# Kernel optimization log

Measured on AMD Instinct MI355X. Metric: run time of the kernel, lower is better.

## Reference

```python
import jax, jax.numpy as jnp
import numpy as np

B, S, D = 1, 2048, 4096
H = 32
Q_RANK, KV_RANK = 1536, 512
NOPE, ROPE, VD = 128, 64, 128
QD = NOPE + ROPE  # 192
EPS = 1e-6
THETA = 10000.0


def setup_inputs() -> dict:
    key = jax.random.key(0)
    ks = jax.random.split(key, 8)
    std = 0.02
    return {
        'hidden_states': jax.random.normal(ks[0], (B, S, D), jnp.float32),
        'Wq_a': jax.random.normal(ks[1], (D, Q_RANK), jnp.float32) * std,
        'q_a_ln_w': jnp.ones((Q_RANK,), jnp.float32),
        'Wq_b': jax.random.normal(ks[2], (Q_RANK, H * QD), jnp.float32) * std,
        'Wkv_a': jax.random.normal(ks[3], (D, KV_RANK + ROPE), jnp.float32) * std,
        'kv_a_ln_w': jnp.ones((KV_RANK,), jnp.float32),
        'Wkv_b': jax.random.normal(ks[4], (KV_RANK, H * (NOPE + VD)), jnp.float32) * std,
        'Wo': jax.random.normal(ks[5], (H * VD, D), jnp.float32) * std,
    }


def _rmsnorm(x, w):
    return x * jax.lax.rsqrt(jnp.mean(x * x, axis=-1, keepdims=True) + EPS) * w


def _rotate_half(x):
    h = x.shape[-1] // 2
    return jnp.concatenate([-x[..., h:], x[..., :h]], axis=-1)


def _apply_rope(x, cos, sin):
    # DeepSeek interleave permutation: view(..., d//2, 2).transpose -> [evens | odds]
    xp = jnp.concatenate([x[..., 0::2], x[..., 1::2]], axis=-1)
    return xp * cos + _rotate_half(xp) * sin


def _mla_forward(hidden_states, Wq_a, q_a_ln_w, Wq_b, Wkv_a, kv_a_ln_w, Wkv_b, Wo):
    b, s, _ = hidden_states.shape
    # low-rank query projection
    q = _rmsnorm(hidden_states @ Wq_a, q_a_ln_w) @ Wq_b          # [b,s,H*QD]
    q = q.reshape(b, s, H, QD).transpose(0, 2, 1, 3)             # [b,H,s,QD]
    q_nope, q_pe = q[..., :NOPE], q[..., NOPE:]
    # compressed kv + shared rope key
    ckv = hidden_states @ Wkv_a                                   # [b,s,KV_RANK+ROPE]
    compressed, k_pe = ckv[..., :KV_RANK], ckv[..., KV_RANK:]
    kv = _rmsnorm(compressed, kv_a_ln_w) @ Wkv_b                 # [b,s,H*(NOPE+VD)]
    kv = kv.reshape(b, s, H, NOPE + VD).transpose(0, 2, 1, 3)    # [b,H,s,NOPE+VD]
    k_nope, v = kv[..., :NOPE], kv[..., NOPE:]
    k_pe = k_pe[:, None, :, :]                                    # [b,1,s,ROPE]
    # rotary tables (cos/sin duplicated halves)
    inv_freq = 1.0 / (THETA ** (jnp.arange(0, ROPE, 2, dtype=jnp.float32) / ROPE))
    freqs = jnp.outer(jnp.arange(s, dtype=jnp.float32), inv_freq)  # [s,ROPE/2]
    emb = jnp.concatenate([freqs, freqs], axis=-1)                 # [s,ROPE]
    cos = jnp.cos(emb)[None, None].astype(hidden_states.dtype)
    sin = jnp.sin(emb)[None, None].astype(hidden_states.dtype)
    q_pe = _apply_rope(q_pe, cos, sin)
    k_pe = _apply_rope(k_pe, cos, sin)
    # assemble full q/k heads
    qf = jnp.concatenate([q_nope, q_pe], axis=-1)                 # [b,H,s,QD]
    kf = jnp.concatenate([k_nope, jnp.broadcast_to(k_pe, (b, H, s, ROPE))], axis=-1)
    scale = QD ** (-0.5)
    scores = jnp.einsum('bhqd,bhkd->bhqk', qf, kf) * scale        # [b,H,s,s]
    causal = jnp.tril(jnp.ones((s, s), dtype=bool))
    scores = jnp.where(causal, scores, jnp.finfo(scores.dtype).min)
    probs = jax.nn.softmax(scores, axis=-1)
    o = jnp.einsum('bhqk,bhkd->bhqd', probs, v)                   # [b,H,s,VD]
    o = o.transpose(0, 2, 1, 3).reshape(b, s, H * VD)
    return o @ Wo


def reference(hidden_states, Wq_a, q_a_ln_w, Wq_b, Wkv_a, kv_a_ln_w, Wkv_b, Wo):
    return _mla_forward(hidden_states, Wq_a, q_a_ln_w, Wq_b, Wkv_a, kv_a_ln_w, Wkv_b, Wo)
```

## Files before the change

### kernel.cpp

```cpp
#include <hip/hip_runtime.h>

typedef unsigned short u16;
using bf16x8 = __attribute__((ext_vector_type(8))) __bf16;
using f32x4  = __attribute__((ext_vector_type(4))) float;
using s16x8  = __attribute__((ext_vector_type(8))) short;
using s16x4  = __attribute__((ext_vector_type(4))) short;

#define AS1 __attribute__((address_space(1)))
#define AS3 __attribute__((address_space(3)))

__device__ __forceinline__ void gload16(const u16* g, u16* l) {
  __builtin_amdgcn_global_load_lds((AS1 void*)(size_t)g, (AS3 void*)l, 16, 0, 0);
}

__device__ __forceinline__ u16 f2bf(float f) {
  unsigned u = __float_as_uint(f);
  u += 0x7fffu + ((u >> 16) & 1u);
  return (u16)(u >> 16);
}
__device__ __forceinline__ float bf2f(u16 h) {
  return __uint_as_float(((unsigned)h) << 16);
}

__device__ __forceinline__ void transpose_tile(const float* __restrict__ W,
                                               u16* __restrict__ WT,
                                               int K, int N, int nb, int kb,
                                               u16 (*tile)[72]) {
  const int t = threadIdx.x;
  const int rr = t >> 3;
  const int cc = (t & 7) * 8;
#pragma unroll
  for (int pass = 0; pass < 2; ++pass) {
    const float* src = W + (size_t)(kb + pass * 32 + rr) * N + nb + cc;
    float4 a = *reinterpret_cast<const float4*>(src);
    float4 b = *reinterpret_cast<const float4*>(src + 4);
    u16* tr = &tile[pass * 32 + rr][cc];
    tr[0] = f2bf(a.x); tr[1] = f2bf(a.y); tr[2] = f2bf(a.z); tr[3] = f2bf(a.w);
    tr[4] = f2bf(b.x); tr[5] = f2bf(b.y); tr[6] = f2bf(b.z); tr[7] = f2bf(b.w);
  }
  __syncthreads();
#pragma unroll
  for (int pass = 0; pass < 2; ++pass) {
    s16x8 v;
#pragma unroll
    for (int j = 0; j < 8; ++j) v[j] = (short)tile[cc + j][pass * 32 + rr];
    *reinterpret_cast<s16x8*>(WT + (size_t)(nb + pass * 32 + rr) * K + kb + cc) = v;
  }
}

__global__ __launch_bounds__(256) void prep_merged_kernel(
    const float* __restrict__ hs, u16* __restrict__ hs_bf,
    const float* __restrict__ Wqa, const float* __restrict__ Wkva, u16* __restrict__ WabT,
    const float* __restrict__ Wqb, u16* __restrict__ WqbT,
    const float* __restrict__ Wkvb, u16* __restrict__ WkvbT,
    const float* __restrict__ Wo, u16* __restrict__ WoT,
    float* __restrict__ cost, float* __restrict__ sint) {
  __shared__ u16 tile[64][72];
  const int bid = blockIdx.x, t = threadIdx.x;
  if (bid < 8192) {
    int i = (bid * 256 + t) * 4;
    float4 v = *reinterpret_cast<const float4*>(hs + i);
    s16x4 o;
    o[0] = (short)f2bf(v.x); o[1] = (short)f2bf(v.y);
    o[2] = (short)f2bf(v.z); o[3] = (short)f2bf(v.w);
    *reinterpret_cast<s16x4*>(hs_bf + i) = o;
  } else if (bid < 9728) {
    int r = bid - 8192;
    transpose_tile(Wqa, WabT, 4096, 1536, (r % 24) * 64, (r / 24) * 64, tile);
  } else if (bid < 10304) {
    int r = bid - 9728;
    transpose_tile(Wkva, WabT + (size_t)1536 * 4096, 4096, 576, (r % 9) * 64, (r / 9) * 64, tile);
  } else if (bid < 12608) {
    int r = bid - 10304;
    transpose_tile(Wqb, WqbT, 1536, 6144, (r % 96) * 64, (r / 96) * 64, tile);
  } else if (bid < 13632) {
    int r = bid - 12608;
    transpose_tile(Wkvb, WkvbT, 512, 8192, (r % 128) * 64, (r / 128) * 64, tile);
  } else if (bid < 17728) {
    int r = bid - 13632;
    transpose_tile(Wo, WoT, 4096, 4096, (r % 64) * 64, (r / 64) * 64, tile);
  } else {
    int idx = (bid - 17728) * 256 + t;
    int pos = idx >> 5, j = idx & 31;
    float inv = __expf(-(float)j * (9.210340371976184f / 32.0f));
    float f = (float)pos * inv;
    cost[idx] = cosf(f);
    sint[idx] = sinf(f);
  }
}

__global__ __launch_bounds__(256) void norms_merged_kernel(const u16* __restrict__ fused,
                                                           const float* __restrict__ qln,
                                                           const float* __restrict__ kvln,
                                                           u16* __restrict__ qan,
                                                           u16* __restrict__ cn) {
  const int bid = blockIdx.x, t = threadIdx.x;
  const int row = bid & 2047;
  const bool is_q = bid < 2048;
  const int R = is_q ? 1536 : 512;
  const u16* xr = fused + (size_t)row * 2112 + (is_q ? 0 : 1536);
  const float* w = is_q ? qln : kvln;
  u16* yr = (is_q ? qan + (size_t)row * 1536 : cn + (size_t)row * 512);
  float ss = 0.f;
  for (int i = t; i < R; i += 256) { float f = bf2f(xr[i]); ss += f * f; }
#pragma unroll
  for (int m = 32; m >= 1; m >>= 1) ss += __shfl_xor(ss, m);
  __shared__ float red[4];
  if ((t & 63) == 0) red[t >> 6] = ss;
  __syncthreads();
  float tot = red[0] + red[1] + red[2] + red[3];
  float r = rsqrtf(tot / (float)R + 1e-6f);
  for (int i = t; i < R; i += 256) yr[i] = f2bf(bf2f(xr[i]) * r * w[i]);
}

__global__ __launch_bounds__(256) void builds_merged_kernel(const u16* __restrict__ q,
                                                            const u16* __restrict__ ckv,
                                                            const float* __restrict__ cost,
                                                            const float* __restrict__ sint,
                                                            u16* __restrict__ qf,
                                                            u16* __restrict__ kf) {
  const int bid = blockIdx.x, t = threadIdx.x;
  if (bid < 6144) {
    int o8 = (bid * 256 + t) * 8;
    const float scale = 0.07216878364870323f;
    int c = (o8 % 192) >> 3;
    int rest = o8 / 192;
    int s = rest & 2047, h = rest >> 11;
    const u16* qrow = q + ((size_t)s * 32 + h) * 192;
    s16x8 out;
    if (c < 16) {
      s16x8 v = *reinterpret_cast<const s16x8*>(qrow + c * 8);
#pragma unroll
      for (int j = 0; j < 8; ++j) out[j] = (short)f2bf(bf2f((u16)v[j]) * scale);
    } else {
      int j0 = c * 8 - 128;
      bool lo = j0 < 32;
      int jj0 = lo ? j0 : j0 - 32;
      s16x8 a = *reinterpret_cast<const s16x8*>(qrow + 128 + 2 * jj0);
      s16x8 b = *reinterpret_cast<const s16x8*>(qrow + 128 + 2 * jj0 + 8);
      float4 c0 = *reinterpret_cast<const float4*>(cost + s * 32 + jj0);
      float4 c1 = *reinterpret_cast<const float4*>(cost + s * 32 + jj0 + 4);
      float4 s0 = *reinterpret_cast<const float4*>(sint + s * 32 + jj0);
      float4 s1 = *reinterpret_cast<const float4*>(sint + s * 32 + jj0 + 4);
      float cs[8] = {c0.x, c0.y, c0.z, c0.w, c1.x, c1.y, c1.z, c1.w};
      float sn[8] = {s0.x, s0.y, s0.z, s0.w, s1.x, s1.y, s1.z, s1.w};
#pragma unroll
      for (int j = 0; j < 8; ++j) {
        float x0 = bf2f((u16)((j < 4) ? a[2 * j] : b[2 * j - 8]));
        float x1 = bf2f((u16)((j < 4) ? a[2 * j + 1] : b[2 * j - 7]));
        float v = lo ? (x0 * cs[j] - x1 * sn[j]) : (x1 * cs[j] + x0 * sn[j]);
        out[j] = (short)f2bf(v * scale);
      }
    }
    *reinterpret_cast<s16x8*>(qf + o8) = out;
  } else {
    int o8 = ((bid - 6144) * 256 + t) * 8;
    int j0 = o8 & 63;
    int rest = o8 >> 6;
    int s = rest & 2047, h = rest >> 11;
    bool lo = j0 < 32;
    int jj0 = lo ? j0 : j0 - 32;
    const u16* crow = ckv + (size_t)s * 2112 + 512;
    s16x8 a = *reinterpret_cast<const s16x8*>(crow + 2 * jj0);
    s16x8 b = *reinterpret_cast<const s16x8*>(crow + 2 * jj0 + 8);
    float4 c0 = *reinterpret_cast<const float4*>(cost + s * 32 + jj0);
    float4 c1 = *reinterpret_cast<const float4*>(cost + s * 32 + jj0 + 4);
    float4 s0 = *reinterpret_cast<const float4*>(sint + s * 32 + jj0);
    float4 s1 = *reinterpret_cast<const float4*>(sint + s * 32 + jj0 + 4);
    float cs[8] = {c0.x, c0.y, c0.z, c0.w, c1.x, c1.y, c1.z, c1.w};
    float sn[8] = {s0.x, s0.y, s0.z, s0.w, s1.x, s1.y, s1.z, s1.w};
    s16x8 out;
#pragma unroll
    for (int j = 0; j < 8; ++j) {
      float x0 = bf2f((u16)((j < 4) ? a[2 * j] : b[2 * j - 8]));
      float x1 = bf2f((u16)((j < 4) ? a[2 * j + 1] : b[2 * j - 7]));
      float v = lo ? (x0 * cs[j] - x1 * sn[j]) : (x1 * cs[j] + x0 * sn[j]);
      out[j] = (short)f2bf(v);
    }
    *reinterpret_cast<s16x8*>(kf + ((size_t)h * 2048 + s) * 192 + 128 + j0) = out;
  }
}

template <int EPI>
__device__ __forceinline__ void gemm_v3_body(const u16* __restrict__ A,
                                             const u16* __restrict__ BT,
                                             void* __restrict__ Cv,
                                             void* __restrict__ Cv2,
                                             int M, int N, int K,
                                             int bx, int by, u16* S) {
  const int t0 = threadIdx.x;
  const int lane = t0 & 63, wave = t0 >> 6;
  const int wr = wave >> 1, wc = wave & 1;
  const int row0 = by * 128, col0 = bx * 128;
  const int lrow = lane & 15, lkg = lane >> 4;

  const int lp = lane ^ ((lane >> 3) & 3);
  const int srow_off = lp >> 2;
  const int skel = (lp & 3) * 8;
  const int c0 = wave * 2, c1 = c0 + 1;
  const int arow_c0 = row0 + c0 * 16 + srow_off;
  const int arow_c1 = row0 + c1 * 16 + srow_off;
  int brow_c0 = col0 + c0 * 16 + srow_off; if (brow_c0 > N - 1) brow_c0 = N - 1;
  int brow_c1 = col0 + c1 * 16 + srow_off; if (brow_c1 > N - 1) brow_c1 = N - 1;

  int aoff[4], boff[4];
#pragma unroll
  for (int m = 0; m < 4; ++m) {
    int r = wr * 64 + m * 16 + lrow;
    int off = r * 32 + lkg * 8;
    aoff[m] = off ^ ((off >> 3) & 0x18);
    r = wc * 64 + m * 16 + lrow;
    off = r * 32 + lkg * 8;
    boff[m] = off ^ ((off >> 3) & 0x18);
  }

  const int NT = K >> 5;

#pragma unroll
  for (int pt = 0; pt < 3; ++pt) {
    u16* ab = &S[pt * 8192];
    const int kb = pt * 32 + skel;
    gload16(A  + (size_t)arow_c0 * K + kb, ab + c0 * 512);
    gload16(A  + (size_t)arow_c1 * K + kb, ab + c1 * 512);
    gload16(BT + (size_t)brow_c0 * K + kb, ab + 4096 + c0 * 512);
    gload16(BT + (size_t)brow_c1 * K + kb, ab + 4096 + c1 * 512);
  }

  f32x4 acc[4][4];
#pragma unroll
  for (int m = 0; m < 4; ++m)
#pragma unroll
    for (int n = 0; n < 4; ++n) acc[m][n] = 0.f;

  for (int t = 0; t < NT; ++t) {
    if (t + 2 < NT)      asm volatile("s_waitcnt vmcnt(8)" ::: "memory");
    else if (t + 1 < NT) asm volatile("s_waitcnt vmcnt(4)" ::: "memory");
    else                 asm volatile("s_waitcnt vmcnt(0)" ::: "memory");
    __builtin_amdgcn_s_barrier();
    __builtin_amdgcn_sched_barrier(0);

    const u16* ab = &S[(t & 3) * 8192];
    bf16x8 af[4], bb[4];
#pragma unroll
    for (int m = 0; m < 4; ++m)
      af[m] = *reinterpret_cast<const bf16x8*>(ab + aoff[m]);
#pragma unroll
    for (int n = 0; n < 4; ++n)
      bb[n] = *reinterpret_cast<const bf16x8*>(ab + 4096 + boff[n]);

    if (t + 3 < NT) {
      u16* sb = &S[((t + 3) & 3) * 8192];
      const int kb = (t + 3) * 32 + skel;
      gload16(A  + (size_t)arow_c0 * K + kb, sb + c0 * 512);
      gload16(A  + (size_t)arow_c1 * K + kb, sb + c1 * 512);
      gload16(BT + (size_t)brow_c0 * K + kb, sb + 4096 + c0 * 512);
      gload16(BT + (size_t)brow_c1 * K + kb, sb + 4096 + c1 * 512);
    }

    __builtin_amdgcn_s_setprio(1);
#pragma unroll
    for (int m = 0; m < 4; ++m)
#pragma unroll
      for (int n = 0; n < 4; ++n)
        acc[m][n] = __builtin_amdgcn_mfma_f32_16x16x32_bf16(af[m], bb[n], acc[m][n], 0, 0, 0);
    __builtin_amdgcn_s_setprio(0);
  }

#pragma unroll
  for (int m = 0; m < 4; ++m) {
#pragma unroll
    for (int n = 0; n < 4; ++n) {
      int col = col0 + wc * 64 + n * 16 + lrow;
      int row = row0 + wr * 64 + m * 16 + lkg * 4;
      if (col < N) {
#pragma unroll
        for (int i = 0; i < 4; ++i) {
          size_t idx = (size_t)(row + i) * N + col;
          if (EPI == 1) ((u16*)Cv)[idx] = f2bf(acc[m][n][i]);
          else          ((float*)Cv)[idx] = acc[m][n][i];
        }
      }
    }
  }
}

template <int EPI>
__global__ __launch_bounds__(256) void gemm_v3_kernel(const u16* __restrict__ A,
                                                      const u16* __restrict__ BT,
                                                      void* __restrict__ Cv,
                                                      void* __restrict__ Cv2,
                                                      int M, int N, int K) {
  __shared__ __align__(16) u16 S[4 * 8192];
  gemm_v3_body<EPI>(A, BT, Cv, Cv2, M, N, K, blockIdx.x, blockIdx.y, S);
}

template <int EPI>
__device__ __forceinline__ void gemm_v4_body(const u16* __restrict__ A,
                                             const u16* __restrict__ BT,
                                             void* __restrict__ Cv,
                                             void* __restrict__ Cv2,
                                             int M, int N, int K,
                                             int bx, int by, u16* S) {
  const int t0 = threadIdx.x;
  const int lane = t0 & 63, wave = t0 >> 6;
  const int wr = wave >> 1, wc = wave & 1;
  const int row0 = by * 128, col0 = bx * 256;
  const int lrow = lane & 15, lkg = lane >> 4;

  const int lp = lane ^ ((lane >> 3) & 3);
  const int srow_off = lp >> 2;
  const int skel = (lp & 3) * 8;

  const int ac0 = wave * 2, ac1 = ac0 + 1;
  const int arow_0 = row0 + ac0 * 16 + srow_off;
  const int arow_1 = row0 + ac1 * 16 + srow_off;
  int brow[4];
#pragma unroll
  for (int j = 0; j < 4; ++j) {
    int r = col0 + (wave * 4 + j) * 16 + srow_off;
    brow[j] = (r > N - 1) ? (N - 1) : r;
  }

  int aoff[4], boff[8];
#pragma unroll
  for (int m = 0; m < 4; ++m) {
    int r = wr * 64 + m * 16 + lrow;
    int off = r * 32 + lkg * 8;
    aoff[m] = off ^ ((off >> 3) & 0x18);
  }
#pragma unroll
  for (int n = 0; n < 8; ++n) {
    int r = wc * 128 + n * 16 + lrow;
    int off = r * 32 + lkg * 8;
    boff[n] = off ^ ((off >> 3) & 0x18);
  }

  const int NT = K >> 5;

#pragma unroll
  for (int pt = 0; pt < 2; ++pt) {
    u16* sb = &S[pt * 12288];
    const int kb = pt * 32 + skel;
    gload16(A + (size_t)arow_0 * K + kb, sb + ac0 * 512);
    gload16(A + (size_t)arow_1 * K + kb, sb + ac1 * 512);
#pragma unroll
    for (int j = 0; j < 4; ++j)
      gload16(BT + (size_t)brow[j] * K + kb, sb + 4096 + (wave * 4 + j) * 512);
  }

  f32x4 acc[4][8];
#pragma unroll
  for (int m = 0; m < 4; ++m)
#pragma unroll
    for (int n = 0; n < 8; ++n) acc[m][n] = 0.f;

  int bufr = 0, bufw = 2;
  for (int t = 0; t < NT; ++t) {
    if (t + 2 < NT) {
      u16* sb = &S[bufw * 12288];
      const int kb = (t + 2) * 32 + skel;
      gload16(A + (size_t)arow_0 * K + kb, sb + ac0 * 512);
      gload16(A + (size_t)arow_1 * K + kb, sb + ac1 * 512);
#pragma unroll
      for (int j = 0; j < 4; ++j)
        gload16(BT + (size_t)brow[j] * K + kb, sb + 4096 + (wave * 4 + j) * 512);
      bufw = (bufw + 1 == 3) ? 0 : bufw + 1;
      asm volatile("s_waitcnt vmcnt(12)" ::: "memory");
    } else if (t + 1 < NT) {
      asm volatile("s_waitcnt vmcnt(6)" ::: "memory");
    } else {
      asm volatile("s_waitcnt vmcnt(0)" ::: "memory");
    }
    __builtin_amdgcn_s_barrier();
    __builtin_amdgcn_sched_barrier(0);

    const u16* ab = &S[bufr * 12288];
    bufr = (bufr + 1 == 3) ? 0 : bufr + 1;
    bf16x8 af[4];
#pragma unroll
    for (int m = 0; m < 4; ++m)
      af[m] = *reinterpret_cast<const bf16x8*>(ab + aoff[m]);

    __builtin_amdgcn_s_setprio(1);
#pragma unroll
    for (int n = 0; n < 8; ++n) {
      bf16x8 bbn = *reinterpret_cast<const bf16x8*>(ab + 4096 + boff[n]);
#pragma unroll
      for (int m = 0; m < 4; ++m)
        acc[m][n] = __builtin_amdgcn_mfma_f32_16x16x32_bf16(af[m], bbn, acc[m][n], 0, 0, 0);
    }
    __builtin_amdgcn_s_setprio(0);
  }

#pragma unroll
  for (int m = 0; m < 4; ++m) {
#pragma unroll
    for (int n = 0; n < 8; ++n) {
      int col = col0 + wc * 128 + n * 16 + lrow;
      int row = row0 + wr * 64 + m * 16 + lkg * 4;
      if (EPI == 2) {
        int d = col & 255, hh = col >> 8;
        if (d < 128) {
          u16* dst = (u16*)Cv + ((size_t)hh * 2048 + row) * 192 + d;
#pragma unroll
          for (int i = 0; i < 4; ++i) dst[(size_t)i * 192] = f2bf(acc[m][n][i]);
        } else {
          s16x4 v;
#pragma unroll
          for (int i = 0; i < 4; ++i) v[i] = (short)f2bf(acc[m][n][i]);
          *reinterpret_cast<s16x4*>((u16*)Cv2 + ((size_t)hh * 128 + (d - 128)) * 2048 + row) = v;
        }
      } else if (col < N) {
#pragma unroll
        for (int i = 0; i < 4; ++i) {
          size_t idx = (size_t)(row + i) * N + col;
          if (EPI == 1) ((u16*)Cv)[idx] = f2bf(acc[m][n][i]);
          else          ((float*)Cv)[idx] = acc[m][n][i];
        }
      }
    }
  }
}

template <int EPI>
__global__ __launch_bounds__(256, 2) void gemm_v4_kernel(const u16* __restrict__ A,
                                                         const u16* __restrict__ BT,
                                                         void* __restrict__ Cv,
                                                         void* __restrict__ Cv2,
                                                         int M, int N, int K) {
  __shared__ __align__(16) u16 S[3 * 12288];
  gemm_v4_body<EPI>(A, BT, Cv, Cv2, M, N, K, blockIdx.x, blockIdx.y, S);
}

__global__ __launch_bounds__(256, 2) void gemm_qkv_kernel(const u16* __restrict__ qan,
                                                          const u16* __restrict__ WqbT,
                                                          u16* __restrict__ qout,
                                                          const u16* __restrict__ cn,
                                                          const u16* __restrict__ WkvbT,
                                                          u16* __restrict__ kfb,
                                                          u16* __restrict__ vTb) {
  __shared__ __align__(16) u16 S[3 * 12288];
  if (blockIdx.z == 0) {
    if (blockIdx.x >= 24) return;
    gemm_v4_body<1>(qan, WqbT, qout, nullptr, 2048, 6144, 1536, blockIdx.x, blockIdx.y, S);
  } else {
    gemm_v4_body<2>(cn, WkvbT, kfb, vTb, 2048, 8192, 512, blockIdx.x, blockIdx.y, S);
  }
}

__global__ __launch_bounds__(256) void mla_attn_kernel(const u16* __restrict__ qf,
                                                       const u16* __restrict__ kf,
                                                       const u16* __restrict__ vT,
                                                       u16* __restrict__ o) {
  const int h = blockIdx.x, pair = blockIdx.y;
  const int t = threadIdx.x, wave = t >> 6, lane = t & 63;
  const int lrow = lane & 15, lkg = lane >> 4;
  __shared__ __align__(16) u16 Kt[2][12 * 512];
  __shared__ __align__(16) u16 Vt[2][8 * 512];
  __shared__ __align__(16) u16 Pl[4][16][36];

  const u16* ksrc[3]; u16 *kdst0[3], *kdst1[3];
#pragma unroll
  for (int i = 0; i < 3; ++i) {
    int c = wave * 3 + i, cg = c / 6, kk = c - cg * 6;
    ksrc[i] = kf + ((size_t)h * 2048 + cg * 16 + lrow) * 192 + kk * 32 + lkg * 8;
    kdst0[i] = &Kt[0][c * 512];
    kdst1[i] = &Kt[1][c * 512];
  }
  const u16* vsrc[2]; u16 *vdst0[2], *vdst1[2];
#pragma unroll
  for (int j = 0; j < 2; ++j) {
    int f = wave * 2 + j;
    vsrc[j] = vT + ((size_t)h * 128 + f * 16 + lrow) * 2048 + lkg * 8;
    vdst0[j] = &Vt[0][f * 512];
    vdst1[j] = &Vt[1][f * 512];
  }

  for (int qq = 0; qq < 2; ++qq) {
    const int qb = qq ? (31 - pair) : pair;
    const int qbase = qb * 64 + wave * 16;

    bf16x8 qfr[6];
    const u16* qrow_ptr = qf + ((size_t)h * 2048 + qbase + lrow) * 192;
#pragma unroll
    for (int kk = 0; kk < 6; ++kk)
      qfr[kk] = *reinterpret_cast<const bf16x8*>(qrow_ptr + kk * 32 + lkg * 8);

    f32x4 acc_o[8];
#pragma unroll
    for (int f = 0; f < 8; ++f) acc_o[f] = 0.f;
    float m_run[4], l_par[4];
#pragma unroll
    for (int i = 0; i < 4; ++i) { m_run[i] = -1e30f; l_par[i] = 0.f; }

    const int nt = 2 * qb + 2;

#pragma unroll
    for (int i = 0; i < 3; ++i) gload16(ksrc[i], kdst0[i]);
#pragma unroll
    for (int j = 0; j < 2; ++j) gload16(vsrc[j], vdst0[j]);

    for (int it = 0; it < nt; ++it) {
      const int kt = it * 32;
      if (it + 1 < nt) {
        const int nb = (it + 1) & 1;
        const size_t kadv = (size_t)(it + 1) * 32 * 192;
        const size_t vadv = (size_t)(it + 1) * 32;
#pragma unroll
        for (int i = 0; i < 3; ++i) gload16(ksrc[i] + kadv, nb ? kdst1[i] : kdst0[i]);
#pragma unroll
        for (int j = 0; j < 2; ++j) gload16(vsrc[j] + vadv, nb ? vdst1[j] : vdst0[j]);
        asm volatile("s_waitcnt vmcnt(5)" ::: "memory");
      } else {
        asm volatile("s_waitcnt vmcnt(0)" ::: "memory");
      }
      __builtin_amdgcn_s_barrier();
      __builtin_amdgcn_sched_barrier(0);

      const u16* Kb = &Kt[it & 1][0];
      const u16* Vb = &Vt[it & 1][0];
      if (kt <= qbase + 15) {
        f32x4 sv[2];
        sv[0] = 0.f; sv[1] = 0.f;
#pragma unroll
        for (int cg = 0; cg < 2; ++cg)
#pragma unroll
          for (int kk = 0; kk < 6; ++kk) {
            bf16x8 kfr = *reinterpret_cast<const bf16x8*>(&Kb[(cg * 6 + kk) * 512 + lane * 8]);
            sv[cg] = __builtin_amdgcn_mfma_f32_16x16x32_bf16(qfr[kk], kfr, sv[cg], 0, 0, 0);
          }
        const int qrow_b = qbase + lkg * 4;
        if (kt + 31 > qbase) {
#pragma unroll
          for (int cg = 0; cg < 2; ++cg) {
            int kvcol = kt + cg * 16 + lrow;
#pragma unroll
            for (int i = 0; i < 4; ++i)
              if (kvcol > qrow_b + i) sv[cg][i] = -__builtin_inff();
          }
        }
        float tmax[4];
#pragma unroll
        for (int i = 0; i < 4; ++i) tmax[i] = fmaxf(sv[0][i], sv[1][i]);
#pragma unroll
        for (int m = 8; m >= 1; m >>= 1)
#pragma unroll
          for (int i = 0; i < 4; ++i) tmax[i] = fmaxf(tmax[i], __shfl_xor(tmax[i], m));
        int need = 0;
#pragma unroll
        for (int i = 0; i < 4; ++i) need |= (tmax[i] > m_run[i] + 8.f) ? 1 : 0;
        if (__any(need)) {
#pragma unroll
          for (int i = 0; i < 4; ++i) {
            float mnew = fmaxf(m_run[i], tmax[i]);
            float alpha = __expf(m_run[i] - mnew);
            m_run[i] = mnew;
            l_par[i] *= alpha;
#pragma unroll
            for (int f = 0; f < 8; ++f) acc_o[f][i] *= alpha;
          }
        }
#pragma unroll
        for (int i = 0; i < 4; ++i) {
          sv[0][i] = __expf(sv[0][i] - m_run[i]);
          sv[1][i] = __expf(sv[1][i] - m_run[i]);
          l_par[i] += sv[0][i] + sv[1][i];
        }
#pragma unroll
        for (int cg = 0; cg < 2; ++cg)
#pragma unroll
          for (int i = 0; i < 4; ++i)
            Pl[wave][lkg * 4 + i][cg * 16 + lrow] = f2bf(sv[cg][i]);
        bf16x8 pf = *reinterpret_cast<const bf16x8*>(&Pl[wave][lrow][lkg * 8]);
#pragma unroll
        for (int f = 0; f < 8; ++f) {
          bf16x8 vfr = *reinterpret_cast<const bf16x8*>(&Vb[f * 512 + lane * 8]);
          acc_o[f] = __builtin_amdgcn_mfma_f32_16x16x32_bf16(pf, vfr, acc_o[f], 0, 0, 0);
        }
      }
      __builtin_amdgcn_sched_barrier(0);
      __builtin_amdgcn_s_barrier();
    }
#pragma unroll
    for (int i = 0; i < 4; ++i)
#pragma unroll
      for (int m = 8; m >= 1; m >>= 1) l_par[i] += __shfl_xor(l_par[i], m);
#pragma unroll
    for (int f = 0; f < 8; ++f)
#pragma unroll
      for (int i = 0; i < 4; ++i) {
        int row = qbase + lkg * 4 + i;
        int col = h * 128 + f * 16 + lrow;
        o[(size_t)row * 4096 + col] = f2bf(acc_o[f][i] / l_par[i]);
      }
  }
}

extern "C" void kernel_launch(void* const* d_in, const int* in_sizes, int n_in,
                              void* d_out, int out_size, void* d_ws, size_t ws_size,
                              hipStream_t stream) {
  (void)in_sizes; (void)n_in; (void)out_size; (void)ws_size;
  const float* hs   = (const float*)d_in[0];
  const float* Wqa  = (const float*)d_in[1];
  const float* qln  = (const float*)d_in[2];
  const float* Wqb  = (const float*)d_in[3];
  const float* Wkva = (const float*)d_in[4];
  const float* kvln = (const float*)d_in[5];
  const float* Wkvb = (const float*)d_in[6];
  const float* Wo   = (const float*)d_in[7];
  float* out = (float*)d_out;

  char* p = (char*)d_ws;
  size_t off = 0;
  auto carve = [&](size_t bytes) {
    char* r = p + off;
    off += (bytes + 255) & ~(size_t)255;
    return r;
  };
  u16* hs_bf = (u16*)carve((size_t)2048 * 4096 * 2);
  u16* WabT  = (u16*)carve((size_t)2112 * 4096 * 2);
  u16* WqbT  = (u16*)carve((size_t)6144 * 1536 * 2);
  u16* WkvbT = (u16*)carve((size_t)8192 * 512 * 2);
  u16* WoT   = (u16*)carve((size_t)4096 * 4096 * 2);
  u16* fused = (u16*)carve((size_t)2048 * 2112 * 2);
  u16* qan   = (u16*)carve((size_t)2048 * 1536 * 2);
  u16* q     = (u16*)carve((size_t)2048 * 6144 * 2);
  u16* cn    = (u16*)carve((size_t)2048 * 512 * 2);
  u16* qfb   = (u16*)carve((size_t)32 * 2048 * 192 * 2);
  u16* kfb   = (u16*)carve((size_t)32 * 2048 * 192 * 2);
  u16* vTb   = (u16*)carve((size_t)32 * 128 * 2048 * 2);
  u16* ob    = (u16*)carve((size_t)2048 * 4096 * 2);
  float* cost = (float*)carve((size_t)65536 * 4);
  float* sint = (float*)carve((size_t)65536 * 4);

  prep_merged_kernel<<<17984, 256, 0, stream>>>(hs, hs_bf, Wqa, Wkva, WabT,
                                                Wqb, WqbT, Wkvb, WkvbT, Wo, WoT,
                                                cost, sint);

  gemm_v3_kernel<1><<<dim3(17, 16), 256, 0, stream>>>(hs_bf, WabT, fused, nullptr, 2048, 2112, 4096);

  norms_merged_kernel<<<4096, 256, 0, stream>>>(fused, qln, kvln, qan, cn);

  gemm_qkv_kernel<<<dim3(32, 16, 2), 256, 0, stream>>>(qan, WqbT, q, cn, WkvbT, kfb, vTb);

  builds_merged_kernel<<<8192, 256, 0, stream>>>(q, fused + 1536, cost, sint, qfb, kfb);

  mla_attn_kernel<<<dim3(32, 16), 256, 0, stream>>>(qfb, kfb, vTb, ob);

  gemm_v4_kernel<0><<<dim3(16, 16), 256, 0, stream>>>(ob, WoT, out, nullptr, 2048, 4096, 4096);
}
```

Before: 399.1 us.

## Enlarge attention KV tile to 64 and single-buffer V with late prefetch

After: 393.3 us (median of 2 runs). No clear change (-1.5%).

```diff
diff --git a/kernel.cpp b/kernel.cpp
--- a/kernel.cpp
+++ b/kernel.cpp
@@ -455,26 +455,12 @@
   const int h = blockIdx.x, pair = blockIdx.y;
   const int t = threadIdx.x, wave = t >> 6, lane = t & 63;
   const int lrow = lane & 15, lkg = lane >> 4;
-  __shared__ __align__(16) u16 Kt[2][12 * 512];
-  __shared__ __align__(16) u16 Vt[2][8 * 512];
-  __shared__ __align__(16) u16 Pl[4][16][36];
-
-  const u16* ksrc[3]; u16 *kdst0[3], *kdst1[3];
-#pragma unroll
-  for (int i = 0; i < 3; ++i) {
-    int c = wave * 3 + i, cg = c / 6, kk = c - cg * 6;
-    ksrc[i] = kf + ((size_t)h * 2048 + cg * 16 + lrow) * 192 + kk * 32 + lkg * 8;
-    kdst0[i] = &Kt[0][c * 512];
-    kdst1[i] = &Kt[1][c * 512];
-  }
-  const u16* vsrc[2]; u16 *vdst0[2], *vdst1[2];
-#pragma unroll
-  for (int j = 0; j < 2; ++j) {
-    int f = wave * 2 + j;
-    vsrc[j] = vT + ((size_t)h * 128 + f * 16 + lrow) * 2048 + lkg * 8;
-    vdst0[j] = &Vt[0][f * 512];
-    vdst1[j] = &Vt[1][f * 512];
-  }
+  __shared__ __align__(16) u16 Kt[2][24 * 512];
+  __shared__ __align__(16) u16 Vt[16 * 512];
+  __shared__ __align__(16) u16 Pl[4][16][72];
+
+  const u16* ksrc0 = kf + ((size_t)h * 2048 + wave * 16 + lrow) * 192 + lkg * 8;
+  const u16* vsrc0 = vT + ((size_t)h * 128 + wave * 32 + lrow) * 2048 + lkg * 8;
 
   for (int qq = 0; qq < 2; ++qq) {
     const int qb = qq ? (31 - pair) : pair;
@@ -493,24 +479,27 @@
 #pragma unroll
     for (int i = 0; i < 4; ++i) { m_run[i] = -1e30f; l_par[i] = 0.f; }
 
-    const int nt = 2 * qb + 2;
-
-#pragma unroll
-    for (int i = 0; i < 3; ++i) gload16(ksrc[i], kdst0[i]);
-#pragma unroll
-    for (int j = 0; j < 2; ++j) gload16(vsrc[j], vdst0[j]);
+    const int nt = qb + 1;
+
+#pragma unroll
+    for (int kk = 0; kk < 6; ++kk)
+      gload16(ksrc0 + kk * 32, &Kt[0][(wave * 6 + kk) * 512]);
+#pragma unroll
+    for (int j = 0; j < 4; ++j) {
+      int fo = (j >> 1), ck = j & 1;
+      gload16(vsrc0 + (size_t)fo * 16 * 2048 + ck * 32,
+              &Vt[((wave * 2 + fo) * 2 + ck) * 512]);
+    }
 
     for (int it = 0; it < nt; ++it) {
-      const int kt = it * 32;
+      const int kt = it * 64;
       if (it + 1 < nt) {
-        const int nb = (it + 1) & 1;
-        const size_t kadv = (size_t)(it + 1) * 32 * 192;
-        const size_t vadv = (size_t)(it + 1) * 32;
-#pragma unroll
-        for (int i = 0; i < 3; ++i) gload16(ksrc[i] + kadv, nb ? kdst1[i] : kdst0[i]);
-#pragma unroll
-        for (int j = 0; j < 2; ++j) gload16(vsrc[j] + vadv, nb ? vdst1[j] : vdst0[j]);
-        asm volatile("s_waitcnt vmcnt(5)" ::: "memory");
+        const u16* ks = ksrc0 + (size_t)(kt + 64) * 192;
+        u16* kd = &Kt[(it + 1) & 1][0];
+#pragma unroll
+        for (int kk = 0; kk < 6; ++kk)
+          gload16(ks + kk * 32, kd + (wave * 6 + kk) * 512);
+        asm volatile("s_waitcnt vmcnt(6)" ::: "memory");
       } else {
         asm volatile("s_waitcnt vmcnt(0)" ::: "memory");
       }
@@ -518,68 +507,80 @@
       __builtin_amdgcn_sched_barrier(0);
 
       const u16* Kb = &Kt[it & 1][0];
-      const u16* Vb = &Vt[it & 1][0];
-      if (kt <= qbase + 15) {
-        f32x4 sv[2];
-        sv[0] = 0.f; sv[1] = 0.f;
-#pragma unroll
-        for (int cg = 0; cg < 2; ++cg)
-#pragma unroll
-          for (int kk = 0; kk < 6; ++kk) {
-            bf16x8 kfr = *reinterpret_cast<const bf16x8*>(&Kb[(cg * 6 + kk) * 512 + lane * 8]);
-            sv[cg] = __builtin_amdgcn_mfma_f32_16x16x32_bf16(qfr[kk], kfr, sv[cg], 0, 0, 0);
-          }
-        const int qrow_b = qbase + lkg * 4;
-        if (kt + 31 > qbase) {
-#pragma unroll
-          for (int cg = 0; cg < 2; ++cg) {
-            int kvcol = kt + cg * 16 + lrow;
-#pragma unroll
-            for (int i = 0; i < 4; ++i)
-              if (kvcol > qrow_b + i) sv[cg][i] = -__builtin_inff();
-          }
-        }
-        float tmax[4];
-#pragma unroll
-        for (int i = 0; i < 4; ++i) tmax[i] = fmaxf(sv[0][i], sv[1][i]);
-#pragma unroll
-        for (int m = 8; m >= 1; m >>= 1)
-#pragma unroll
-          for (int i = 0; i < 4; ++i) tmax[i] = fmaxf(tmax[i], __shfl_xor(tmax[i], m));
-        int need = 0;
-#pragma unroll
-        for (int i = 0; i < 4; ++i) need |= (tmax[i] > m_run[i] + 8.f) ? 1 : 0;
-        if (__any(need)) {
-#pragma unroll
-          for (int i = 0; i < 4; ++i) {
-            float mnew = fmaxf(m_run[i], tmax[i]);
-            float alpha = __expf(m_run[i] - mnew);
-            m_run[i] = mnew;
-            l_par[i] *= alpha;
-#pragma unroll
-            for (int f = 0; f < 8; ++f) acc_o[f][i] *= alpha;
-          }
-        }
+      f32x4 sv[4];
+#pragma unroll
+      for (int cg = 0; cg < 4; ++cg) sv[cg] = 0.f;
+#pragma unroll
+      for (int cg = 0; cg < 4; ++cg)
+#pragma unroll
+        for (int kk = 0; kk < 6; ++kk) {
+          bf16x8 kfr = *reinterpret_cast<const bf16x8*>(&Kb[(cg * 6 + kk) * 512 + lane * 8]);
+          sv[cg] = __builtin_amdgcn_mfma_f32_16x16x32_bf16(qfr[kk], kfr, sv[cg], 0, 0, 0);
+        }
+
+      const int qrow_b = qbase + lkg * 4;
+      if (it + 1 == nt) {
+#pragma unroll
+        for (int cg = 0; cg < 4; ++cg) {
+          int kvcol = kt + cg * 16 + lrow;
+#pragma unroll
+          for (int i = 0; i < 4; ++i)
+            if (kvcol > qrow_b + i) sv[cg][i] = -__builtin_inff();
+        }
+      }
+      float tmax[4];
+#pragma unroll
+      for (int i = 0; i < 4; ++i)
+        tmax[i] = fmaxf(fmaxf(sv[0][i], sv[1][i]), fmaxf(sv[2][i], sv[3][i]));
+#pragma unroll
+      for (int m = 8; m >= 1; m >>= 1)
+#pragma unroll
+        for (int i = 0; i < 4; ++i) tmax[i] = fmaxf(tmax[i], __shfl_xor(tmax[i], m));
+      int need = 0;
+#pragma unroll
+      for (int i = 0; i < 4; ++i) need |= (tmax[i] > m_run[i] + 8.f) ? 1 : 0;
+      if (__any(need)) {
 #pragma unroll
         for (int i = 0; i < 4; ++i) {
-          sv[0][i] = __expf(sv[0][i] - m_run[i]);
-          sv[1][i] = __expf(sv[1][i] - m_run[i]);
-          l_par[i] += sv[0][i] + sv[1][i];
-        }
-#pragma unroll
-        for (int cg = 0; cg < 2; ++cg)
-#pragma unroll
-          for (int i = 0; i < 4; ++i)
-            Pl[wave][lkg * 4 + i][cg * 16 + lrow] = f2bf(sv[cg][i]);
-        bf16x8 pf = *reinterpret_cast<const bf16x8*>(&Pl[wave][lrow][lkg * 8]);
+          float mnew = fmaxf(m_run[i], tmax[i]);
+          float alpha = __expf(m_run[i] - mnew);
+          m_run[i] = mnew;
+          l_par[i] *= alpha;
+#pragma unroll
+          for (int f = 0; f < 8; ++f) acc_o[f][i] *= alpha;
+        }
+      }
+#pragma unroll
+      for (int i = 0; i < 4; ++i) {
+#pragma unroll
+        for (int cg = 0; cg < 4; ++cg) sv[cg][i] = __expf(sv[cg][i] - m_run[i]);
+        l_par[i] += (sv[0][i] + sv[1][i]) + (sv[2][i] + sv[3][i]);
+      }
+#pragma unroll
+      for (int cg = 0; cg < 4; ++cg)
+#pragma unroll
+        for (int i = 0; i < 4; ++i)
+          Pl[wave][lkg * 4 + i][cg * 16 + lrow] = f2bf(sv[cg][i]);
+#pragma unroll
+      for (int ck = 0; ck < 2; ++ck) {
+        bf16x8 pf = *reinterpret_cast<const bf16x8*>(&Pl[wave][lrow][ck * 32 + lkg * 8]);
 #pragma unroll
         for (int f = 0; f < 8; ++f) {
-          bf16x8 vfr = *reinterpret_cast<const bf16x8*>(&Vb[f * 512 + lane * 8]);
+          bf16x8 vfr = *reinterpret_cast<const bf16x8*>(&Vt[(f * 2 + ck) * 512 + lane * 8]);
           acc_o[f] = __builtin_amdgcn_mfma_f32_16x16x32_bf16(pf, vfr, acc_o[f], 0, 0, 0);
         }
       }
       __builtin_amdgcn_sched_barrier(0);
       __builtin_amdgcn_s_barrier();
+      if (it + 1 < nt) {
+        const u16* vs = vsrc0 + kt + 64;
+#pragma unroll
+        for (int j = 0; j < 4; ++j) {
+          int fo = (j >> 1), ck = j & 1;
+          gload16(vs + (size_t)fo * 16 * 2048 + ck * 32,
+                  &Vt[((wave * 2 + fo) * 2 + ck) * 512]);
+        }
+      }
     }
 #pragma unroll
     for (int i = 0; i < 4; ++i)
```
